# Kernel tuning notes

Measured on AMD Instinct MI355X. Metric: run time of the kernel, lower is better.

## Reference

```python
import jax, jax.numpy as jnp
import numpy as np

N = 8192
D_IN, D_MID, D_EMB = 1024, 256, 64
N_EDGES = N * 8


def setup_inputs() -> dict:
    key = jax.random.key(0)
    ks = jax.random.split(key, 6)
    X = jax.random.normal(ks[0], (N, D_IN), dtype=jnp.float32)
    # Xavier-uniform style init as in get_weight_initial
    b1 = np.sqrt(6.0 / (D_IN + D_MID))
    b2 = np.sqrt(6.0 / (D_MID + D_EMB))
    W1 = jax.random.uniform(ks[1], (D_IN, D_MID), minval=-b1, maxval=b1, dtype=jnp.float32)
    W2 = jax.random.uniform(ks[2], (D_MID, D_EMB), minval=-b2, maxval=b2, dtype=jnp.float32)
    edge_val = jax.random.uniform(ks[3], (N_EDGES,), dtype=jnp.float32)
    edge_src = jax.random.randint(ks[4], (N_EDGES,), 0, N, dtype=jnp.int32)
    edge_dst = jax.random.randint(ks[5], (N_EDGES,), 0, N, dtype=jnp.int32)
    return {"X": X, "W1": W1, "W2": W2, "edge_val": edge_val,
            "edge_src": edge_src, "edge_dst": edge_dst}


def reference(X, W1, W2, edge_val, edge_src, edge_dst):
    n = X.shape[0]

    def spmm(H):  # sparse Laplacian (COO) times dense H
        return jax.ops.segment_sum(edge_val[:, None] * H[edge_src], edge_dst,
                                   num_segments=n)

    h = jax.nn.relu(spmm(X @ W1))          # [N, D_MID]
    emb = spmm(h @ W2)                      # [N, D_EMB]
    # pairwise squared Euclidean distances between rows of emb -> [N, N]
    sq = jnp.sum(emb * emb, axis=1)
    dist = sq[:, None] + sq[None, :] - 2.0 * (emb @ emb.T)
    recons_w = jax.nn.softmax(-dist, axis=1) + 1e-10
    return recons_w
```

## Files before the change

kernel.cpp:

```cpp
#include <hip/hip_runtime.h>
#include <cstddef>

constexpr int NN     = 8192;
constexpr int DIN    = 1024;
constexpr int DMID   = 256;
constexpr int DEMB   = 64;
constexpr int NEDGE  = 65536;
constexpr int MAXDEG = 64;

typedef __attribute__((ext_vector_type(8))) short bf16x8;
typedef __attribute__((ext_vector_type(4))) float f32x4;
#define MFMA16(a, b, c) __builtin_amdgcn_mfma_f32_16x16x32_bf16((a), (b), (c), 0, 0, 0)

constexpr float LOG2E    = 1.44269504088896340736f;
constexpr float TWOLOG2E = 2.88539008177792681472f;

__device__ __forceinline__ unsigned short bf16_rne(float x) {
  unsigned u = __float_as_uint(x);
  return (unsigned short)((u + 0x7FFFu + ((u >> 16) & 1u)) >> 16);
}
__device__ __forceinline__ float bf16_tof(unsigned short h) {
  return __uint_as_float((unsigned)h << 16);
}

constexpr int WCONV_BLOCKS = (DMID * DIN + DEMB * DMID) / 256;
constexpr int XCONV_BLOCKS = NN * DIN / (256 * 8);
constexpr int ZERO_BLOCKS  = 16;
__global__ __launch_bounds__(256) void prep_kernel(const float* __restrict__ W1,
                                                   const float* __restrict__ W2,
                                                   const float* __restrict__ X,
                                                   unsigned short* __restrict__ W1b,
                                                   unsigned short* __restrict__ W2b,
                                                   unsigned short* __restrict__ Xb,
                                                   int* __restrict__ zero_base)
{
  int b = blockIdx.x;
  if (b < WCONV_BLOCKS) {
    int idx = b * 256 + threadIdx.x;
    if (idx < DMID * DIN) {
      int n = idx >> 10, k = idx & 1023;
      W1b[idx] = bf16_rne(W1[k * DMID + n]);
    } else {
      int t = idx - DMID * DIN;
      int n = t >> 8, k = t & 255;
      W2b[t] = bf16_rne(W2[k * DEMB + n]);
    }
  } else if (b < WCONV_BLOCKS + XCONV_BLOCKS) {
    int idx = (b - WCONV_BLOCKS) * 2048 + threadIdx.x * 8;
    float4 x0 = *(const float4*)(X + idx);
    float4 x1 = *(const float4*)(X + idx + 4);
    bf16x8 h;
    h[0] = (short)bf16_rne(x0.x); h[1] = (short)bf16_rne(x0.y);
    h[2] = (short)bf16_rne(x0.z); h[3] = (short)bf16_rne(x0.w);
    h[4] = (short)bf16_rne(x1.x); h[5] = (short)bf16_rne(x1.y);
    h[6] = (short)bf16_rne(x1.z); h[7] = (short)bf16_rne(x1.w);
    *(bf16x8*)(Xb + idx) = h;
  } else {
    int idx = (b - WCONV_BLOCKS - XCONV_BLOCKS) * 1024 + threadIdx.x * 4;
    *(int4*)(zero_base + idx) = make_int4(0, 0, 0, 0);
  }
}

__global__ __launch_bounds__(256) void build_ell_kernel(
    const int* __restrict__ esrc, const float* __restrict__ ev,
    const int* __restrict__ edst, int* __restrict__ cursor,
    int* __restrict__ ell_src, float* __restrict__ ell_val)
{
  int e = blockIdx.x * 256 + threadIdx.x;
  int d = edst[e];
  int pos = atomicAdd(&cursor[d], 1);
  if (pos < MAXDEG) {
    ell_src[d * MAXDEG + pos] = esrc[e];
    ell_val[d * MAXDEG + pos] = ev[e];
  }
}

__global__ __launch_bounds__(256) void gemm1_kernel(
    const unsigned short* __restrict__ Xb, const unsigned short* __restrict__ W1b,
    unsigned short* __restrict__ G1)
{
  const int lane = threadIdx.x & 63;
  const int wave = threadIdx.x >> 6;
  const int m0 = blockIdx.x * 64 + wave * 16;
  const int n0 = blockIdx.y * 64;
  const int rl = lane & 15;
  const int kq = (lane >> 4) * 8;
  f32x4 zero = {0.f, 0.f, 0.f, 0.f};
  f32x4 acc[4] = {zero, zero, zero, zero};
  for (int s = 0; s < DIN / 32; ++s) {
    const int kb = s * 32 + kq;
    bf16x8 ah = *(const bf16x8*)(Xb + (size_t)(m0 + rl) * DIN + kb);
#pragma unroll
    for (int ns = 0; ns < 4; ++ns) {
      bf16x8 bh = *(const bf16x8*)(W1b + (size_t)(n0 + ns * 16 + rl) * DIN + kb);
      acc[ns] = MFMA16(ah, bh, acc[ns]);
    }
  }
  const int rq = (lane >> 4) * 4;
#pragma unroll
  for (int ns = 0; ns < 4; ++ns)
#pragma unroll
    for (int r = 0; r < 4; ++r)
      G1[(size_t)(m0 + rq + r) * DMID + n0 + ns * 16 + rl] = bf16_rne(acc[ns][r]);
}

__global__ __launch_bounds__(256) void spmm1_gemm2_kernel(
    const unsigned short* __restrict__ G1, const int* __restrict__ deg,
    const int* __restrict__ ell_src, const float* __restrict__ ell_val,
    const unsigned short* __restrict__ W2b, float* __restrict__ E1)
{
  __shared__ unsigned short Hs[16][DMID + 8];
  const int lane = threadIdx.x & 63;
  const int wave = threadIdx.x >> 6;
  const int r0 = blockIdx.x * 16;
  const int c = lane * 4;
#pragma unroll
  for (int rr = 0; rr < 4; ++rr) {
    const int row = wave * 4 + rr;
    const int r = r0 + row;
    const int dg = min(deg[r], MAXDEG);
    const int* sp = ell_src + (size_t)r * MAXDEG;
    const float* vp = ell_val + (size_t)r * MAXDEG;
    float4 acc = make_float4(0.f, 0.f, 0.f, 0.f);
    for (int e = 0; e < dg; ++e) {
      const int s = sp[e];
      const float v = vp[e];
      ushort4 h = *(const ushort4*)(G1 + (size_t)s * DMID + c);
      acc.x = fmaf(v, bf16_tof(h.x), acc.x);
      acc.y = fmaf(v, bf16_tof(h.y), acc.y);
      acc.z = fmaf(v, bf16_tof(h.z), acc.z);
      acc.w = fmaf(v, bf16_tof(h.w), acc.w);
    }
    ushort4 hq;
    hq.x = bf16_rne(fmaxf(acc.x, 0.f));
    hq.y = bf16_rne(fmaxf(acc.y, 0.f));
    hq.z = bf16_rne(fmaxf(acc.z, 0.f));
    hq.w = bf16_rne(fmaxf(acc.w, 0.f));
    *(ushort4*)(&Hs[row][c]) = hq;
  }
  __syncthreads();
  const int rl = lane & 15;
  const int kq = (lane >> 4) * 8;
  f32x4 acc4 = {0.f, 0.f, 0.f, 0.f};
#pragma unroll
  for (int s = 0; s < DMID / 32; ++s) {
    const int kb = s * 32 + kq;
    bf16x8 a = *(const bf16x8*)(&Hs[rl][kb]);
    bf16x8 b = *(const bf16x8*)(W2b + (size_t)(wave * 16 + rl) * DMID + kb);
    acc4 = MFMA16(a, b, acc4);
  }
  const int rq = (lane >> 4) * 4;
#pragma unroll
  for (int r = 0; r < 4; ++r)
    E1[(size_t)(r0 + rq + r) * DEMB + wave * 16 + rl] = acc4[r];
}

__global__ __launch_bounds__(256) void spmm2_kernel(
    const float* __restrict__ H, const int* __restrict__ deg,
    const int* __restrict__ ell_src, const float* __restrict__ ell_val,
    unsigned short* __restrict__ EmbH, float* __restrict__ sqv)
{
  const int lane = threadIdx.x & 63;
  const int wave = threadIdx.x >> 6;
  const int r = blockIdx.x * 4 + wave;
  const int dg = min(deg[r], MAXDEG);
  const int* sp = ell_src + (size_t)r * MAXDEG;
  const float* vp = ell_val + (size_t)r * MAXDEG;
  float acc = 0.f;
  for (int e = 0; e < dg; ++e)
    acc = fmaf(vp[e], H[(size_t)sp[e] * DEMB + lane], acc);
  unsigned short h = bf16_rne(acc);
  EmbH[(size_t)r * DEMB + lane] = h;
  float hf = bf16_tof(h);
  float sq = hf * hf;
#pragma unroll
  for (int off = 32; off; off >>= 1) sq += __shfl_xor(sq, off, 64);
  if (lane == 0) sqv[r] = sq * LOG2E;
}

__device__ __forceinline__ void dist_tile_32(
    const unsigned short* __restrict__ EH, int ibase, int jbase, int lane,
    f32x4 (&acc)[4][2])
{
  const int rl = lane & 15;
  const int kq = (lane >> 4) * 8;
#pragma unroll
  for (int s = 0; s < 2; ++s) {
    const int kb = s * 32 + kq;
    bf16x8 a[4], b[2];
#pragma unroll
    for (int t = 0; t < 4; ++t)
      a[t] = *(const bf16x8*)(EH + (size_t)(ibase + t * 16 + rl) * DEMB + kb);
#pragma unroll
    for (int t = 0; t < 2; ++t)
      b[t] = *(const bf16x8*)(EH + (size_t)(jbase + t * 16 + rl) * DEMB + kb);
#pragma unroll
    for (int ms = 0; ms < 4; ++ms)
#pragma unroll
      for (int ns = 0; ns < 2; ++ns)
        acc[ms][ns] = MFMA16(a[ms], b[ns], acc[ms][ns]);
  }
}

__global__ __launch_bounds__(256, 4) void rowsum_kernel(
    const unsigned short* __restrict__ EH, const float* __restrict__ sq,
    float* __restrict__ rowsum)
{
  const int lane = threadIdx.x & 63;
  const int wave = threadIdx.x >> 6;
  const int wr = wave >> 1, wc = wave & 1;
  const int ibase = blockIdx.y * 128 + wr * 64;
  const int rl = lane & 15;
  const int rq = (lane >> 4) * 4;

  float si[4][4];
#pragma unroll
  for (int ms = 0; ms < 4; ++ms)
#pragma unroll
    for (int r = 0; r < 4; ++r) si[ms][r] = sq[ibase + ms * 16 + rq + r];

  float rs[4][4] = {};
  for (int jt = 0; jt < 8; ++jt) {
    const int jbase = blockIdx.x * 512 + jt * 64 + wc * 32;
    float sj[2];
#pragma unroll
    for (int ns = 0; ns < 2; ++ns) sj[ns] = sq[jbase + ns * 16 + rl];
    f32x4 zero = {0.f, 0.f, 0.f, 0.f};
    f32x4 acc[4][2];
#pragma unroll
    for (int ms = 0; ms < 4; ++ms)
#pragma unroll
      for (int ns = 0; ns < 2; ++ns) acc[ms][ns] = zero;
    dist_tile_32(EH, ibase, jbase, lane, acc);
#pragma unroll
    for (int ms = 0; ms < 4; ++ms)
#pragma unroll
      for (int ns = 0; ns < 2; ++ns)
#pragma unroll
        for (int r = 0; r < 4; ++r)
          rs[ms][r] += __builtin_exp2f(
              fmaf(TWOLOG2E, acc[ms][ns][r], -si[ms][r] - sj[ns]));
  }
#pragma unroll
  for (int ms = 0; ms < 4; ++ms)
#pragma unroll
    for (int r = 0; r < 4; ++r) {
      float v = rs[ms][r];
      v += __shfl_xor(v, 1, 64);
      v += __shfl_xor(v, 2, 64);
      v += __shfl_xor(v, 4, 64);
      v += __shfl_xor(v, 8, 64);
      if (rl == 0) atomicAdd(&rowsum[ibase + ms * 16 + rq + r], v);
    }
}

__global__ __launch_bounds__(256, 4) void dist_write_kernel(
    const unsigned short* __restrict__ EH, const float* __restrict__ sq,
    const float* __restrict__ rowsum, float* __restrict__ out)
{
  const int lane = threadIdx.x & 63;
  const int wave = threadIdx.x >> 6;
  const int wr = wave >> 1, wc = wave & 1;
  const int ibase = blockIdx.y * 128 + wr * 64;
  const int jbase = blockIdx.x * 64 + wc * 32;
  const int rl = lane & 15;
  const int rq = (lane >> 4) * 4;

  f32x4 zero = {0.f, 0.f, 0.f, 0.f};
  f32x4 acc[4][2];
#pragma unroll
  for (int ms = 0; ms < 4; ++ms)
#pragma unroll
    for (int ns = 0; ns < 2; ++ns) acc[ms][ns] = zero;
  dist_tile_32(EH, ibase, jbase, lane, acc);

  float si[4][4], ri[4][4], sj[2];
#pragma unroll
  for (int ms = 0; ms < 4; ++ms)
#pragma unroll
    for (int r = 0; r < 4; ++r) {
      const int i = ibase + ms * 16 + rq + r;
      si[ms][r] = sq[i];
      ri[ms][r] = 1.f / rowsum[i];
    }
#pragma unroll
  for (int ns = 0; ns < 2; ++ns) sj[ns] = sq[jbase + ns * 16 + rl];

#pragma unroll
  for (int ms = 0; ms < 4; ++ms)
#pragma unroll
    for (int r = 0; r < 4; ++r) {
      const size_t row = (size_t)(ibase + ms * 16 + rq + r) * NN;
#pragma unroll
      for (int ns = 0; ns < 2; ++ns) {
        float e = __builtin_exp2f(
            fmaf(TWOLOG2E, acc[ms][ns][r], -si[ms][r] - sj[ns]));
        __builtin_nontemporal_store(fmaf(e, ri[ms][r], 1e-10f),
                                    &out[row + jbase + ns * 16 + rl]);
      }
    }
}

extern "C" void kernel_launch(void* const* d_in, const int* in_sizes, int n_in,
                              void* d_out, int out_size, void* d_ws, size_t ws_size,
                              hipStream_t stream)
{
  const float* X  = (const float*)d_in[0];
  const float* W1 = (const float*)d_in[1];
  const float* W2 = (const float*)d_in[2];
  const float* ev = (const float*)d_in[3];
  const int* esrc = (const int*)d_in[4];
  const int* edst = (const int*)d_in[5];
  float* out = (float*)d_out;

  char* p = (char*)d_ws;
  auto alloc = [&](size_t bytes) { char* q = p; p += (bytes + 255) & ~(size_t)255; return q; };

  int*   cursor  = (int*)alloc(NN * 4);
  float* rowsum  = (float*)alloc(NN * 4);
  float* sqv     = (float*)alloc(NN * 4);
  float* E1      = (float*)alloc((size_t)NN * DEMB * 4);
  unsigned short* W1b  = (unsigned short*)alloc((size_t)DMID * DIN * 2);
  unsigned short* W2b  = (unsigned short*)alloc((size_t)DEMB * DMID * 2);
  unsigned short* Xb   = (unsigned short*)alloc((size_t)NN * DIN * 2);
  unsigned short* G1   = (unsigned short*)alloc((size_t)NN * DMID * 2);
  unsigned short* EmbH = (unsigned short*)alloc((size_t)NN * DEMB * 2);
  int*   ell_src = (int*)alloc((size_t)NN * MAXDEG * 4);
  float* ell_val = (float*)alloc((size_t)NN * MAXDEG * 4);

  prep_kernel<<<WCONV_BLOCKS + XCONV_BLOCKS + ZERO_BLOCKS, 256, 0, stream>>>(
      W1, W2, X, W1b, W2b, Xb, cursor);
  build_ell_kernel<<<NEDGE / 256, 256, 0, stream>>>(esrc, ev, edst, cursor,
                                                    ell_src, ell_val);

  gemm1_kernel<<<dim3(NN / 64, DMID / 64), 256, 0, stream>>>(Xb, W1b, G1);
  spmm1_gemm2_kernel<<<NN / 16, 256, 0, stream>>>(G1, cursor, ell_src, ell_val,
                                                  W2b, E1);
  spmm2_kernel<<<NN / 4, 256, 0, stream>>>(E1, cursor, ell_src, ell_val, EmbH, sqv);

  rowsum_kernel<<<dim3(NN / 512, NN / 128), 256, 0, stream>>>(EmbH, sqv, rowsum);
  dist_write_kernel<<<dim3(NN / 64, NN / 128), 256, 0, stream>>>(EmbH, sqv, rowsum,
                                                                 out);
}
```

Baseline: 439.5 us.

## Fuse rowsum and distance-write kernels into persistent kernel with grid barrier

```diff
diff --git a/kernel.cpp b/kernel.cpp
--- a/kernel.cpp
+++ b/kernel.cpp
@@ -25,7 +25,7 @@
 
 constexpr int WCONV_BLOCKS = (DMID * DIN + DEMB * DMID) / 256;
 constexpr int XCONV_BLOCKS = NN * DIN / (256 * 8);
-constexpr int ZERO_BLOCKS  = 16;
+constexpr int ZERO_BLOCKS  = 17;
 __global__ __launch_bounds__(256) void prep_kernel(const float* __restrict__ W1,
                                                    const float* __restrict__ W2,
                                                    const float* __restrict__ X,
@@ -178,6 +178,20 @@
   if (lane == 0) sqv[r] = sq * LOG2E;
 }
 
+__device__ __forceinline__ void gsync(int* bar, int phase) {
+  __syncthreads();
+  if (threadIdx.x == 0) {
+    __threadfence();
+    atomicAdd(bar, 1);
+    const int target = phase * (int)gridDim.x;
+    while (__hip_atomic_load(bar, __ATOMIC_RELAXED, __HIP_MEMORY_SCOPE_AGENT)
+           < target)
+      __builtin_amdgcn_s_sleep(2);
+    __threadfence();
+  }
+  __syncthreads();
+}
+
 __device__ __forceinline__ void dist_tile_32(
     const unsigned short* __restrict__ EH, int ibase, int jbase, int lane,
     f32x4 (&acc)[4][2])
@@ -202,29 +216,68 @@
   }
 }
 
-__global__ __launch_bounds__(256, 4) void rowsum_kernel(
+__global__ __launch_bounds__(256, 4) void dist_fused_kernel(
     const unsigned short* __restrict__ EH, const float* __restrict__ sq,
-    float* __restrict__ rowsum)
+    float* __restrict__ rowsum, float* __restrict__ out, int* bar)
 {
   const int lane = threadIdx.x & 63;
   const int wave = threadIdx.x >> 6;
   const int wr = wave >> 1, wc = wave & 1;
-  const int ibase = blockIdx.y * 128 + wr * 64;
   const int rl = lane & 15;
   const int rq = (lane >> 4) * 4;
 
-  float si[4][4];
-#pragma unroll
-  for (int ms = 0; ms < 4; ++ms)
-#pragma unroll
-    for (int r = 0; r < 4; ++r) si[ms][r] = sq[ibase + ms * 16 + rq + r];
-
-  float rs[4][4] = {};
-  for (int jt = 0; jt < 8; ++jt) {
-    const int jbase = blockIdx.x * 512 + jt * 64 + wc * 32;
-    float sj[2];
-#pragma unroll
-    for (int ns = 0; ns < 2; ++ns) sj[ns] = sq[jbase + ns * 16 + rl];
+  for (int vb = blockIdx.x; vb < 16 * (NN / 128); vb += gridDim.x) {
+    const int by = vb >> 4, bx = vb & 15;
+    const int ibase = by * 128 + wr * 64;
+
+    float si[4][4];
+#pragma unroll
+    for (int ms = 0; ms < 4; ++ms)
+#pragma unroll
+      for (int r = 0; r < 4; ++r) si[ms][r] = sq[ibase + ms * 16 + rq + r];
+
+    float rs[4][4] = {};
+    for (int jt = 0; jt < 8; ++jt) {
+      const int jbase = bx * 512 + jt * 64 + wc * 32;
+      float sj[2];
+#pragma unroll
+      for (int ns = 0; ns < 2; ++ns) sj[ns] = sq[jbase + ns * 16 + rl];
+      f32x4 zero = {0.f, 0.f, 0.f, 0.f};
+      f32x4 acc[4][2];
+#pragma unroll
+      for (int ms = 0; ms < 4; ++ms)
+#pragma unroll
+        for (int ns = 0; ns < 2; ++ns) acc[ms][ns] = zero;
+      dist_tile_32(EH, ibase, jbase, lane, acc);
+#pragma unroll
+      for (int ms = 0; ms < 4; ++ms)
+#pragma unroll
+        for (int ns = 0; ns < 2; ++ns)
+#pragma unroll
+          for (int r = 0; r < 4; ++r)
+            rs[ms][r] += __builtin_exp2f(
+                fmaf(TWOLOG2E, acc[ms][ns][r], -si[ms][r] - sj[ns]));
+    }
+#pragma unroll
+    for (int ms = 0; ms < 4; ++ms)
+#pragma unroll
+      for (int r = 0; r < 4; ++r) {
+        float v = rs[ms][r];
+        v += __shfl_xor(v, 1, 64);
+        v += __shfl_xor(v, 2, 64);
+        v += __shfl_xor(v, 4, 64);
+        v += __shfl_xor(v, 8, 64);
+        if (rl == 0) atomicAdd(&rowsum[ibase + ms * 16 + rq + r], v);
+      }
+  }
+
+  gsync(bar, 1);
+
+  for (int vb = blockIdx.x; vb < (NN / 64) * (NN / 128); vb += gridDim.x) {
+    const int bj = vb & 127, bi = vb >> 7;
+    const int ibase = bi * 128 + wr * 64;
+    const int jbase = bj * 64 + wc * 32;
+
     f32x4 zero = {0.f, 0.f, 0.f, 0.f};
     f32x4 acc[4][2];
 #pragma unroll
@@ -232,73 +285,33 @@
 #pragma unroll
       for (int ns = 0; ns < 2; ++ns) acc[ms][ns] = zero;
     dist_tile_32(EH, ibase, jbase, lane, acc);
-#pragma unroll
-    for (int ms = 0; ms < 4; ++ms)
-#pragma unroll
-      for (int ns = 0; ns < 2; ++ns)
-#pragma unroll
-        for (int r = 0; r < 4; ++r)
-          rs[ms][r] += __builtin_exp2f(
+
+    float si[4][4], ri[4][4], sj[2];
+#pragma unroll
+    for (int ms = 0; ms < 4; ++ms)
+#pragma unroll
+      for (int r = 0; r < 4; ++r) {
+        const int i = ibase + ms * 16 + rq + r;
+        si[ms][r] = sq[i];
+        ri[ms][r] = 1.f / rowsum[i];
+      }
+#pragma unroll
+    for (int ns = 0; ns < 2; ++ns) sj[ns] = sq[jbase + ns * 16 + rl];
+
+#pragma unroll
+    for (int ms = 0; ms < 4; ++ms)
+#pragma unroll
+      for (int r = 0; r < 4; ++r) {
+        const size_t row = (size_t)(ibase + ms * 16 + rq + r) * NN;
+#pragma unroll
+        for (int ns = 0; ns < 2; ++ns) {
+          float e = __builtin_exp2f(
               fmaf(TWOLOG2E, acc[ms][ns][r], -si[ms][r] - sj[ns]));
-  }
-#pragma unroll
-  for (int ms = 0; ms < 4; ++ms)
-#pragma unroll
-    for (int r = 0; r < 4; ++r) {
-      float v = rs[ms][r];
-      v += __shfl_xor(v, 1, 64);
-      v += __shfl_xor(v, 2, 64);
-      v += __shfl_xor(v, 4, 64);
-      v += __shfl_xor(v, 8, 64);
-      if (rl == 0) atomicAdd(&rowsum[ibase + ms * 16 + rq + r], v);
-    }
-}
-
-__global__ __launch_bounds__(256, 4) void dist_write_kernel(
-    const unsigned short* __restrict__ EH, const float* __restrict__ sq,
-    const float* __restrict__ rowsum, float* __restrict__ out)
-{
-  const int lane = threadIdx.x & 63;
-  const int wave = threadIdx.x >> 6;
-  const int wr = wave >> 1, wc = wave & 1;
-  const int ibase = blockIdx.y * 128 + wr * 64;
-  const int jbase = blockIdx.x * 64 + wc * 32;
-  const int rl = lane & 15;
-  const int rq = (lane >> 4) * 4;
-
-  f32x4 zero = {0.f, 0.f, 0.f, 0.f};
-  f32x4 acc[4][2];
-#pragma unroll
-  for (int ms = 0; ms < 4; ++ms)
-#pragma unroll
-    for (int ns = 0; ns < 2; ++ns) acc[ms][ns] = zero;
-  dist_tile_32(EH, ibase, jbase, lane, acc);
-
-  float si[4][4], ri[4][4], sj[2];
-#pragma unroll
-  for (int ms = 0; ms < 4; ++ms)
-#pragma unroll
-    for (int r = 0; r < 4; ++r) {
-      const int i = ibase + ms * 16 + rq + r;
-      si[ms][r] = sq[i];
-      ri[ms][r] = 1.f / rowsum[i];
-    }
-#pragma unroll
-  for (int ns = 0; ns < 2; ++ns) sj[ns] = sq[jbase + ns * 16 + rl];
-
-#pragma unroll
-  for (int ms = 0; ms < 4; ++ms)
-#pragma unroll
-    for (int r = 0; r < 4; ++r) {
-      const size_t row = (size_t)(ibase + ms * 16 + rq + r) * NN;
-#pragma unroll
-      for (int ns = 0; ns < 2; ++ns) {
-        float e = __builtin_exp2f(
-            fmaf(TWOLOG2E, acc[ms][ns][r], -si[ms][r] - sj[ns]));
-        __builtin_nontemporal_store(fmaf(e, ri[ms][r], 1e-10f),
-                                    &out[row + jbase + ns * 16 + rl]);
+          __builtin_nontemporal_store(fmaf(e, ri[ms][r], 1e-10f),
+                                      &out[row + jbase + ns * 16 + rl]);
+        }
       }
-    }
+  }
 }
 
 extern "C" void kernel_launch(void* const* d_in, const int* in_sizes, int n_in,
@@ -318,6 +331,7 @@
 
   int*   cursor  = (int*)alloc(NN * 4);
   float* rowsum  = (float*)alloc(NN * 4);
+  int*   bar     = (int*)alloc(4096);
   float* sqv     = (float*)alloc(NN * 4);
   float* E1      = (float*)alloc((size_t)NN * DEMB * 4);
   unsigned short* W1b  = (unsigned short*)alloc((size_t)DMID * DIN * 2);
@@ -338,7 +352,12 @@
                                                   W2b, E1);
   spmm2_kernel<<<NN / 4, 256, 0, stream>>>(E1, cursor, ell_src, ell_val, EmbH, sqv);
 
-  rowsum_kernel<<<dim3(NN / 512, NN / 128), 256, 0, stream>>>(EmbH, sqv, rowsum);
-  dist_write_kernel<<<dim3(NN / 64, NN / 128), 256, 0, stream>>>(EmbH, sqv, rowsum,
-                                                                 out);
-}
+  int occ = 0;
+  if (hipOccupancyMaxActiveBlocksPerMultiprocessor(&occ, dist_fused_kernel, 256, 0)
+      != hipSuccess || occ < 1)
+    occ = 1;
+  int grid = occ * 256;
+  if (grid > 1024) grid = 1024;
+
+  dist_fused_kernel<<<grid, 256, 0, stream>>>(EmbH, sqv, rowsum, out, bar);
+}
```

Measured after the change: 491.8 us. 11.9% more time.
